# Performance work log

Hardware: AMD Instinct MI355X
Metric: run time of the kernel (lower is better)

## Reference

```python
import jax, jax.numpy as jnp
import numpy as np

EMBED_DIM = 1024
NUM_HEADS = 16
HEAD_DIM = EMBED_DIM // NUM_HEADS


def setup_inputs() -> dict:
    key = jax.random.key(0)
    k_x, k_qw, k_qb, k_ow, k_ob = jax.random.split(key, 5)
    C = EMBED_DIM
    # torch nn.Linear init scale ~ U(-1/sqrt(fan_in), 1/sqrt(fan_in)); use small normals
    s = 1.0 / np.sqrt(C)
    return {
        "x": jax.random.normal(k_x, (4, 2048, C), dtype=jnp.float32),
        "qkv_w": jax.random.uniform(k_qw, (3 * C, C), jnp.float32, -s, s),
        "qkv_b": jax.random.uniform(k_qb, (3 * C,), jnp.float32, -s, s),
        "fc_w": jax.random.uniform(k_ow, (C, C), jnp.float32, -s, s),
        "fc_b": jax.random.uniform(k_ob, (C,), jnp.float32, -s, s),
    }


def reference(x, qkv_w, qkv_b, fc_w, fc_b):
    B, N, C = x.shape
    H, D = NUM_HEADS, HEAD_DIM
    scale = D ** -0.5
    qkv = x @ qkv_w.T + qkv_b                      # [B,N,3C]
    qkv = qkv.reshape(B, N, 3, H, D)
    q, k, v = [jnp.transpose(qkv[:, :, i], (0, 2, 1, 3)) for i in range(3)]  # [B,H,N,D]
    attn = jnp.einsum("bhqd,bhkd->bhqk", q, k) * scale
    attn = jax.nn.softmax(attn, axis=-1)
    out = jnp.einsum("bhqk,bhkd->bhqd", attn, v)   # [B,H,N,D]
    out = jnp.transpose(out, (0, 2, 1, 3)).reshape(B, N, C)
    return out @ fc_w.T + fc_b
```

## Files before the change

kernel.cpp:

```cpp
#include <hip/hip_runtime.h>

#define NUM_HEADS 16
#define HEAD_DIM  64
#define EMB       1024
#define SEQ       2048
#define BATCH     4
#define MROWS     (BATCH * SEQ)
#define QKV_ELEMS (MROWS * EMB)

typedef __attribute__((ext_vector_type(4)))  float  floatx4;
typedef __attribute__((ext_vector_type(16))) float  floatx16;
typedef __attribute__((ext_vector_type(8)))  __bf16 bf16x8;

__device__ __forceinline__ unsigned short f2bf(float f) {
    unsigned int u = __float_as_uint(f);
    u += 0x7fffu + ((u >> 16) & 1u);
    return (unsigned short)(u >> 16);
}

__device__ __forceinline__ ushort4 pk4(float4 v) {
    return make_ushort4(f2bf(v.x), f2bf(v.y), f2bf(v.z), f2bf(v.w));
}

__device__ __forceinline__ uint2 packbf4t(float a0, float a1, float a2, float a3) {
    uint2 r;
    r.x = __builtin_amdgcn_perm(__float_as_uint(a1), __float_as_uint(a0), 0x07060302u);
    r.y = __builtin_amdgcn_perm(__float_as_uint(a3), __float_as_uint(a2), 0x07060302u);
    return r;
}

__device__ __forceinline__ bf16x8 mk8(uint2 lo, uint2 hi) {
    union { uint4 u; bf16x8 b; } cvt;
    cvt.u = make_uint4(lo.x, lo.y, hi.x, hi.y);
    return cvt.b;
}

__device__ __forceinline__ float truncbf(float f) {
    return __uint_as_float(__float_as_uint(f) & 0xffff0000u);
}

#define MFMA16(a, b, c) __builtin_amdgcn_mfma_f32_16x16x32_bf16((a), (b), (c), 0, 0, 0)
#define MFMA32(a, b, c) __builtin_amdgcn_mfma_f32_32x32x16_bf16((a), (b), (c), 0, 0, 0)
#define EXP2(x) __builtin_amdgcn_exp2f(x)

__device__ __forceinline__ void async16(const unsigned short* g, unsigned short* l) {
    __builtin_amdgcn_global_load_lds((const __attribute__((address_space(1))) void*)g,
                                     (__attribute__((address_space(3))) void*)l,
                                     16, 0, 0);
}


#define QSCALE 0.18033688011112042f

#define XV4  2097152
#define QWV4 786432
#define FWV4 262144

__global__ __launch_bounds__(256)
void convert_kernel(const float* __restrict__ x, const float* __restrict__ qw,
                    const float* __restrict__ fw,
                    unsigned short* __restrict__ xb, unsigned short* __restrict__ qwb,
                    unsigned short* __restrict__ fwb)
{
    const size_t i = (size_t)blockIdx.x * 256 + threadIdx.x;
    const float* src; unsigned short* dst; size_t off;
    if (i < XV4)              { src = x;  dst = xb;  off = i; }
    else if (i < XV4 + QWV4)  { src = qw; dst = qwb; off = i - XV4; }
    else                      { src = fw; dst = fwb; off = i - (XV4 + QWV4); }
    float4 v = ((const float4*)src)[off];
    ((ushort4*)dst)[off] = pk4(v);
}

__global__ __launch_bounds__(256, 3)
void qkv_kernel(const unsigned short* __restrict__ X, const unsigned short* __restrict__ W,
                const float* __restrict__ BIAS,
                unsigned short* __restrict__ qb, unsigned short* __restrict__ kb,
                unsigned short* __restrict__ vtb)
{
    __shared__ unsigned short As[128 * 32];
    __shared__ unsigned short Bs[128 * 32];

    const int t    = threadIdx.x;
    const int n0   = blockIdx.x * 128;
    const int m0   = blockIdx.y * 128;
    const int wave = t >> 6, lane = t & 63;
    const int wm   = wave & 1, wn = wave >> 1;
    const int l15  = lane & 15, quad = lane >> 4;

    const int srow = wave * 32 + (lane >> 2);
    const int scol = (lane & 3) * 8;
    const int gcol = (((lane & 3) - ((lane >> 3) & 3)) & 3) * 8;
    const unsigned short* gA = X + (size_t)(m0 + srow) * EMB + gcol;
    const unsigned short* gB = W + (size_t)(n0 + srow) * EMB + gcol;
    unsigned short* lA = &As[srow * 32 + scol];
    unsigned short* lB = &Bs[srow * 32 + scol];

    const int arot = (l15 >> 1) & 3;

    const floatx4 zero4 = {0.f, 0.f, 0.f, 0.f};
    floatx4 acc[4][4];
    #pragma unroll
    for (int i = 0; i < 4; ++i)
        #pragma unroll
        for (int j = 0; j < 4; ++j) acc[i][j] = zero4;

    for (int k0 = 0; k0 < EMB; k0 += 32) {
        __syncthreads();
        async16(gA + k0,                     lA);
        async16(gA + k0 + (size_t)16 * EMB,  lA + 16 * 32);
        async16(gB + k0,                     lB);
        async16(gB + k0 + (size_t)16 * EMB,  lB + 16 * 32);
        __syncthreads();

        bf16x8 af[4], bfv[4];
        #pragma unroll
        for (int i = 0; i < 4; ++i) {
            const int pc = ((quad + arot) & 3) * 8;
            af[i]  = *(const bf16x8*)&As[(wm * 64 + i * 16 + l15) * 32 + pc];
            bfv[i] = *(const bf16x8*)&Bs[(wn * 64 + i * 16 + l15) * 32 + pc];
        }
        #pragma unroll
        for (int mi = 0; mi < 4; ++mi)
            #pragma unroll
            for (int ni = 0; ni < 4; ++ni)
                acc[mi][ni] = MFMA16(af[mi], bfv[ni], acc[mi][ni]);
    }

    const int bb = m0 >> 11;
    #pragma unroll
    for (int ni = 0; ni < 4; ++ni) {
        const int gc     = n0 + wn * 64 + ni * 16 + l15;
        const float bias = BIAS[gc];
        const int which  = gc >> 10;
        const int rem    = gc & 1023;
        const int hh     = rem >> 6;
        const int dd     = rem & 63;
        #pragma unroll
        for (int mi = 0; mi < 4; ++mi) {
            const int nseq0 = (m0 & 2047) + wm * 64 + mi * 16 + quad * 4;
            floatx4 v = acc[mi][ni];
            if (which == 2) {
                ushort4 pk;
                pk.x = f2bf(v[0] + bias); pk.y = f2bf(v[1] + bias);
                pk.z = f2bf(v[2] + bias); pk.w = f2bf(v[3] + bias);
                *(ushort4*)&vtb[((size_t)(bb * NUM_HEADS + hh) * HEAD_DIM + dd) * SEQ + nseq0] = pk;
            } else {
                unsigned short* dst = which ? kb : qb;
                const float sc = which ? 1.0f : QSCALE;
                #pragma unroll
                for (int r = 0; r < 4; ++r)
                    dst[((size_t)(bb * NUM_HEADS + hh) * SEQ + (nseq0 + r)) * HEAD_DIM + dd] =
                        f2bf((v[r] + bias) * sc);
            }
        }
    }
}

__global__ __launch_bounds__(512, 4)
void attn_kernel(const unsigned short* __restrict__ qb, const unsigned short* __restrict__ kb,
                 const unsigned short* __restrict__ vtb, unsigned short* __restrict__ attnb)
{
    __shared__ unsigned short smem[16384];

    const int t    = threadIdx.x;
    const int bh   = blockIdx.x;
    const int q0   = blockIdx.y * 256;
    const int b    = bh >> 4, hh = bh & 15;
    const int wave = t >> 6, lane = t & 63;
    const int l31  = lane & 31, hl = lane >> 5;
    const int srow = lane >> 2;
    const int scol = (lane & 3) * 8;
    const int gcol = (((lane & 3) - ((lane >> 3) & 3)) & 3) * 8;
    const int rrot = (l31 >> 1) & 3;

    const unsigned short* qp = qb  + (size_t)bh * SEQ * HEAD_DIM;
    const unsigned short* kp = kb  + (size_t)bh * SEQ * HEAD_DIM;
    const unsigned short* vp = vtb + (size_t)bh * HEAD_DIM * SEQ;

    {
        const int qr = wave * 16 + srow;
        #pragma unroll
        for (int s = 0; s < 2; ++s)
            #pragma unroll
            for (int h = 0; h < 2; ++h)
                async16(qp + (size_t)(q0 + s * 128 + qr) * 64 + h * 32 + gcol,
                        &smem[s * 8192 + h * 4096 + qr * 32 + scol]);
    }
    __syncthreads();
    bf16x8 qf[4];
    #pragma unroll
    for (int ks = 0; ks < 4; ++ks)
        qf[ks] = *(const bf16x8*)&smem[(wave >> 2) * 8192 + (ks >> 1) * 4096 +
                 ((wave & 3) * 32 + l31) * 32 + ((((ks & 1) * 2 + hl) + rrot) & 3) * 8];

    floatx16 o[2];
    #pragma unroll
    for (int i = 0; i < 16; ++i) { o[0][i] = 0.f; o[1][i] = 0.f; }
    float dsum = 0.f;

    for (int kv0 = 0; kv0 < SEQ; kv0 += 128) {
        __syncthreads();
        {
            const int kr = wave * 16 + srow;
            async16(kp + (size_t)(kv0 + kr) * 64 + gcol,      &smem[kr * 32 + scol]);
            async16(kp + (size_t)(kv0 + kr) * 64 + 32 + gcol, &smem[4096 + kr * 32 + scol]);
            const int kk = wave >> 1;
            #pragma unroll
            for (int j = 0; j < 2; ++j) {
                const int vd = (wave & 1) * 32 + j * 16 + srow;
                async16(vp + (size_t)vd * SEQ + kv0 + kk * 32 + gcol,
                        &smem[8192 + kk * 2048 + vd * 32 + scol]);
            }
        }
        __syncthreads();

        #pragma unroll
        for (int tt = 0; tt < 4; ++tt) {
            floatx16 st;
            #pragma unroll
            for (int i = 0; i < 16; ++i) st[i] = 0.f;
            __builtin_amdgcn_s_setprio(1);
            #pragma unroll
            for (int ks = 0; ks < 4; ++ks) {
                bf16x8 kf = *(const bf16x8*)&smem[(ks >> 1) * 4096 +
                            (tt * 32 + l31) * 32 + ((((ks & 1) * 2 + hl) + rrot) & 3) * 8];
                st = MFMA32(kf, qf[ks], st);
            }
            __builtin_amdgcn_s_setprio(0);

            float ev[16];
            #pragma unroll
            for (int i = 0; i < 16; ++i) ev[i] = EXP2(st[i]);

            {
                float t0  = truncbf(ev[0]),  t1  = truncbf(ev[1]);
                float t2  = truncbf(ev[2]),  t3  = truncbf(ev[3]);
                float t4  = truncbf(ev[4]),  t5  = truncbf(ev[5]);
                float t6  = truncbf(ev[6]),  t7  = truncbf(ev[7]);
                float t8  = truncbf(ev[8]),  t9  = truncbf(ev[9]);
                float t10 = truncbf(ev[10]), t11 = truncbf(ev[11]);
                float t12 = truncbf(ev[12]), t13 = truncbf(ev[13]);
                float t14 = truncbf(ev[14]), t15 = truncbf(ev[15]);
                dsum += (((t0 + t1) + (t2 + t3)) + ((t4 + t5) + (t6 + t7))) +
                        (((t8 + t9) + (t10 + t11)) + ((t12 + t13) + (t14 + t15)));
            }

            uint2 pk0 = packbf4t(ev[0],  ev[1],  ev[2],  ev[3]);
            uint2 pk1 = packbf4t(ev[4],  ev[5],  ev[6],  ev[7]);
            uint2 pk2 = packbf4t(ev[8],  ev[9],  ev[10], ev[11]);
            uint2 pk3 = packbf4t(ev[12], ev[13], ev[14], ev[15]);

            auto sA0 = __builtin_amdgcn_permlane32_swap(pk0.x, pk1.x, false, false);
            auto sA1 = __builtin_amdgcn_permlane32_swap(pk0.y, pk1.y, false, false);
            auto sB0 = __builtin_amdgcn_permlane32_swap(pk2.x, pk3.x, false, false);
            auto sB1 = __builtin_amdgcn_permlane32_swap(pk2.y, pk3.y, false, false);
            bf16x8 pfA = mk8(make_uint2(sA0[0], sA1[0]), make_uint2(sA0[1], sA1[1]));
            bf16x8 pfB = mk8(make_uint2(sB0[0], sB1[0]), make_uint2(sB0[1], sB1[1]));

            __builtin_amdgcn_s_setprio(1);
            #pragma unroll
            for (int s = 0; s < 2; ++s) {
                const bf16x8 pf = s ? pfB : pfA;
                const int kvblk = tt * 2 + s;
                const int vbase = 8192 + (kvblk >> 1) * 2048;
                const int vchun = ((((kvblk & 1) * 2 + hl) + rrot) & 3) * 8;
                #pragma unroll
                for (int dt = 0; dt < 2; ++dt) {
                    bf16x8 vf = *(const bf16x8*)&smem[vbase + (dt * 32 + l31) * 32 + vchun];
                    o[dt] = MFMA32(pf, vf, o[dt]);
                }
            }
            __builtin_amdgcn_s_setprio(0);
        }
    }

    float dtot = dsum + __shfl_xor(dsum, 32);

    #pragma unroll
    for (int g = 0; g < 4; ++g)
        #pragma unroll
        for (int e = 0; e < 4; ++e) {
            const float da  = __shfl(dtot, g * 8 + e);
            const float db  = __shfl(dtot, g * 8 + e + 4);
            const float inv = 1.0f / (hl ? db : da);
            const int  qrow = q0 + wave * 32 + e + g * 8 + hl * 4;
            #pragma unroll
            for (int dt = 0; dt < 2; ++dt)
                attnb[(size_t)(b * SEQ + qrow) * EMB + hh * HEAD_DIM + dt * 32 + l31] =
                    f2bf(o[dt][g * 4 + e] * inv);
        }
}

__global__ __launch_bounds__(256, 3)
void proj_kernel(const unsigned short* __restrict__ A, const unsigned short* __restrict__ W,
                 const float* __restrict__ BIAS, float* __restrict__ out)
{
    __shared__ unsigned short As[128 * 32];
    __shared__ unsigned short Bs[128 * 32];

    const int t    = threadIdx.x;
    const int n0   = blockIdx.x * 128;
    const int m0   = blockIdx.y * 128;
    const int wave = t >> 6, lane = t & 63;
    const int wm   = wave & 1, wn = wave >> 1;
    const int l15  = lane & 15, quad = lane >> 4;

    const int srow = wave * 32 + (lane >> 2);
    const int scol = (lane & 3) * 8;
    const int gcol = (((lane & 3) - ((lane >> 3) & 3)) & 3) * 8;
    const unsigned short* gA = A + (size_t)(m0 + srow) * EMB + gcol;
    const unsigned short* gB = W + (size_t)(n0 + srow) * EMB + gcol;
    unsigned short* lA = &As[srow * 32 + scol];
    unsigned short* lB = &Bs[srow * 32 + scol];

    const int arot = (l15 >> 1) & 3;

    const floatx4 zero4 = {0.f, 0.f, 0.f, 0.f};
    floatx4 acc[4][4];
    #pragma unroll
    for (int i = 0; i < 4; ++i)
        #pragma unroll
        for (int j = 0; j < 4; ++j) acc[i][j] = zero4;

    for (int k0 = 0; k0 < EMB; k0 += 32) {
        __syncthreads();
        async16(gA + k0,                     lA);
        async16(gA + k0 + (size_t)16 * EMB,  lA + 16 * 32);
        async16(gB + k0,                     lB);
        async16(gB + k0 + (size_t)16 * EMB,  lB + 16 * 32);
        __syncthreads();

        bf16x8 af[4], bfv[4];
        #pragma unroll
        for (int i = 0; i < 4; ++i) {
            const int pc = ((quad + arot) & 3) * 8;
            af[i]  = *(const bf16x8*)&As[(wm * 64 + i * 16 + l15) * 32 + pc];
            bfv[i] = *(const bf16x8*)&Bs[(wn * 64 + i * 16 + l15) * 32 + pc];
        }
        #pragma unroll
        for (int mi = 0; mi < 4; ++mi)
            #pragma unroll
            for (int ni = 0; ni < 4; ++ni)
                acc[mi][ni] = MFMA16(af[mi], bfv[ni], acc[mi][ni]);
    }

    #pragma unroll
    for (int ni = 0; ni < 4; ++ni) {
        const int gc     = n0 + wn * 64 + ni * 16 + l15;
        const float bias = BIAS[gc];
        #pragma unroll
        for (int mi = 0; mi < 4; ++mi) {
            const int gm = m0 + wm * 64 + mi * 16 + quad * 4;
            #pragma unroll
            for (int r = 0; r < 4; ++r)
                out[(size_t)(gm + r) * EMB + gc] = acc[mi][ni][r] + bias;
        }
    }
}

extern "C" void kernel_launch(void* const* d_in, const int* in_sizes, int n_in,
                              void* d_out, int out_size, void* d_ws, size_t ws_size,
                              hipStream_t stream) {
    (void)in_sizes; (void)n_in; (void)out_size; (void)ws_size;
    const float* x     = (const float*)d_in[0];
    const float* qkv_w = (const float*)d_in[1];
    const float* qkv_b = (const float*)d_in[2];
    const float* fc_w  = (const float*)d_in[3];
    const float* fc_b  = (const float*)d_in[4];
    float* out = (float*)d_out;

    unsigned short* xb    = (unsigned short*)d_ws;
    unsigned short* attnb = xb;
    unsigned short* qbuf  = xb    + QKV_ELEMS;
    unsigned short* kbuf  = qbuf  + QKV_ELEMS;
    unsigned short* vtbuf = kbuf  + QKV_ELEMS;
    unsigned short* qwb   = vtbuf + QKV_ELEMS;
    unsigned short* fwb   = qwb   + 3 * EMB * EMB;

    convert_kernel<<<dim3((XV4 + QWV4 + FWV4) / 256), 256, 0, stream>>>(
        x, qkv_w, fc_w, xb, qwb, fwb);
    qkv_kernel<<<dim3(24, 64), 256, 0, stream>>>(xb, qwb, qkv_b, qbuf, kbuf, vtbuf);
    attn_kernel<<<dim3(64, 8), 512, 0, stream>>>(qbuf, kbuf, vtbuf, attnb);
    proj_kernel<<<dim3(8, 64), 256, 0, stream>>>(attnb, fwb, fc_b, out);
}
```

Before: 269.4 us.

## Double-buffer K/V tiles in attention with async prefetch and manual waitcnt barriers

Doubles the attention kernel's shared-memory buffer so the next 128-row K/V tile is issued via global_load_lds while the current tile is consumed. Explicit vmcnt/lgkmcnt waits and raw s_barrier replace the two __syncthreads per iteration. Q is staged in the second buffer alongside the first K/V tile. The aim is to hide global load latency behind MFMA and exp work. The cost is doubled LDS per block (64 KB), which may reduce occupancy below the launch-bounds target of 4 blocks.

Result: faster. 263.8 us (-2.1%).

```diff
diff --git a/kernel.cpp b/kernel.cpp
--- a/kernel.cpp
+++ b/kernel.cpp
@@ -42,6 +42,8 @@
 #define MFMA16(a, b, c) __builtin_amdgcn_mfma_f32_16x16x32_bf16((a), (b), (c), 0, 0, 0)
 #define MFMA32(a, b, c) __builtin_amdgcn_mfma_f32_32x32x16_bf16((a), (b), (c), 0, 0, 0)
 #define EXP2(x) __builtin_amdgcn_exp2f(x)
+
+#define BAR() asm volatile("s_barrier" ::: "memory")
 
 __device__ __forceinline__ void async16(const unsigned short* g, unsigned short* l) {
     __builtin_amdgcn_global_load_lds((const __attribute__((address_space(1))) void*)g,
@@ -160,7 +162,7 @@
 void attn_kernel(const unsigned short* __restrict__ qb, const unsigned short* __restrict__ kb,
                  const unsigned short* __restrict__ vtb, unsigned short* __restrict__ attnb)
 {
-    __shared__ unsigned short smem[16384];
+    __shared__ unsigned short smem[2][16384];
 
     const int t    = threadIdx.x;
     const int bh   = blockIdx.x;
@@ -177,6 +179,19 @@
     const unsigned short* kp = kb  + (size_t)bh * SEQ * HEAD_DIM;
     const unsigned short* vp = vtb + (size_t)bh * HEAD_DIM * SEQ;
 
+    auto stage_kv = [&](int kv0n, unsigned short* B) {
+        const int kr = wave * 16 + srow;
+        async16(kp + (size_t)(kv0n + kr) * 64 + gcol,      &B[kr * 32 + scol]);
+        async16(kp + (size_t)(kv0n + kr) * 64 + 32 + gcol, &B[4096 + kr * 32 + scol]);
+        const int kk = wave >> 1;
+        #pragma unroll
+        for (int j = 0; j < 2; ++j) {
+            const int vd = (wave & 1) * 32 + j * 16 + srow;
+            async16(vp + (size_t)vd * SEQ + kv0n + kk * 32 + gcol,
+                    &B[8192 + kk * 2048 + vd * 32 + scol]);
+        }
+    };
+
     {
         const int qr = wave * 16 + srow;
         #pragma unroll
@@ -184,35 +199,35 @@
             #pragma unroll
             for (int h = 0; h < 2; ++h)
                 async16(qp + (size_t)(q0 + s * 128 + qr) * 64 + h * 32 + gcol,
-                        &smem[s * 8192 + h * 4096 + qr * 32 + scol]);
-    }
-    __syncthreads();
+                        &smem[1][s * 8192 + h * 4096 + qr * 32 + scol]);
+        stage_kv(0, smem[0]);
+    }
+    asm volatile("s_waitcnt vmcnt(4)" ::: "memory");
+    BAR();
     bf16x8 qf[4];
     #pragma unroll
     for (int ks = 0; ks < 4; ++ks)
-        qf[ks] = *(const bf16x8*)&smem[(wave >> 2) * 8192 + (ks >> 1) * 4096 +
+        qf[ks] = *(const bf16x8*)&smem[1][(wave >> 2) * 8192 + (ks >> 1) * 4096 +
                  ((wave & 3) * 32 + l31) * 32 + ((((ks & 1) * 2 + hl) + rrot) & 3) * 8];
+    asm volatile("s_waitcnt lgkmcnt(0)" ::: "memory");
+    BAR();
 
     floatx16 o[2];
     #pragma unroll
     for (int i = 0; i < 16; ++i) { o[0][i] = 0.f; o[1][i] = 0.f; }
     float dsum = 0.f;
 
-    for (int kv0 = 0; kv0 < SEQ; kv0 += 128) {
-        __syncthreads();
-        {
-            const int kr = wave * 16 + srow;
-            async16(kp + (size_t)(kv0 + kr) * 64 + gcol,      &smem[kr * 32 + scol]);
-            async16(kp + (size_t)(kv0 + kr) * 64 + 32 + gcol, &smem[4096 + kr * 32 + scol]);
-            const int kk = wave >> 1;
-            #pragma unroll
-            for (int j = 0; j < 2; ++j) {
-                const int vd = (wave & 1) * 32 + j * 16 + srow;
-                async16(vp + (size_t)vd * SEQ + kv0 + kk * 32 + gcol,
-                        &smem[8192 + kk * 2048 + vd * 32 + scol]);
-            }
-        }
-        __syncthreads();
+    for (int it = 0; it < 16; ++it) {
+        const int cur = it & 1;
+        if (it < 15) {
+            stage_kv((it + 1) * 128, (unsigned short*)smem[cur ^ 1]);
+            asm volatile("s_waitcnt vmcnt(4)" ::: "memory");
+        } else {
+            asm volatile("s_waitcnt vmcnt(0)" ::: "memory");
+        }
+        BAR();
+
+        const unsigned short* S = smem[cur];
 
         #pragma unroll
         for (int tt = 0; tt < 4; ++tt) {
@@ -222,7 +237,7 @@
             __builtin_amdgcn_s_setprio(1);
             #pragma unroll
             for (int ks = 0; ks < 4; ++ks) {
-                bf16x8 kf = *(const bf16x8*)&smem[(ks >> 1) * 4096 +
+                bf16x8 kf = *(const bf16x8*)&S[(ks >> 1) * 4096 +
                             (tt * 32 + l31) * 32 + ((((ks & 1) * 2 + hl) + rrot) & 3) * 8];
                 st = MFMA32(kf, qf[ks], st);
             }
@@ -266,12 +281,15 @@
                 const int vchun = ((((kvblk & 1) * 2 + hl) + rrot) & 3) * 8;
                 #pragma unroll
                 for (int dt = 0; dt < 2; ++dt) {
-                    bf16x8 vf = *(const bf16x8*)&smem[vbase + (dt * 32 + l31) * 32 + vchun];
+                    bf16x8 vf = *(const bf16x8*)&S[vbase + (dt * 32 + l31) * 32 + vchun];
                     o[dt] = MFMA32(pf, vf, o[dt]);
                 }
             }
             __builtin_amdgcn_s_setprio(0);
         }
+
+        asm volatile("s_waitcnt lgkmcnt(0)" ::: "memory");
+        BAR();
     }
 
     float dtot = dsum + __shfl_xor(dsum, 32);
```
